# Kernel optimization log

Hardware: AMD Instinct MI355X
Metric: run time of the kernel (lower is better)

The kernel has to match this reference:

```python
import jax, jax.numpy as jnp
import numpy as np

E = 500000       # number of temporal edges
D = 128          # in_feats
DOUT = 128       # out_feats
N_NODES = 50000  # destination node vocabulary


def setup_inputs() -> dict:
    key = jax.random.key(0)
    k = jax.random.split(key, 6)
    src_feat = jax.random.normal(k[0], (E, D), jnp.float32)
    dst_feat = jax.random.normal(k[1], (E, D), jnp.float32)
    # edges sorted by destination node (and implicitly by timestamp within each bucket)
    dst = jnp.sort(jax.random.randint(k[2], (E,), 0, N_NODES))
    W_self = jax.random.normal(k[3], (D, DOUT), jnp.float32) / np.sqrt(D).astype(np.float32)
    b_self = jnp.zeros((DOUT,), jnp.float32)
    W_neigh = jax.random.normal(k[4], (D, DOUT), jnp.float32) / np.sqrt(D).astype(np.float32)
    b_neigh = jnp.zeros((DOUT,), jnp.float32)
    return dict(src_feat=src_feat, dst_feat=dst_feat, dst=dst,
                W_self=W_self, b_self=b_self, W_neigh=W_neigh, b_neigh=b_neigh)


def _segment_cummean(feat, dst):
    """Cumulative mean of `feat` within contiguous buckets of equal `dst`.

    Equivalent to DGL group_apply_edges(group_by='dst') with the 'mean' branch:
    h_feat = cumsum(h_neighs, dim=1) / (deg_index + 1) on the ragged buckets.
    """
    En = feat.shape[0]
    idx = jnp.arange(En)
    is_start = jnp.concatenate([jnp.ones((1,), bool), dst[1:] != dst[:-1]])
    # running max propagates each bucket's start index to all of its edges
    start_idx = jax.lax.associative_scan(jnp.maximum, jnp.where(is_start, idx, 0))
    cs = jnp.cumsum(feat, axis=0)  # [E, D] global prefix sum
    base = jnp.where((start_idx > 0)[:, None],
                     cs[jnp.maximum(start_idx - 1, 0)], jnp.float32(0.0))
    seg_cs = cs - base                       # within-bucket inclusive cumsum
    pos = (idx - start_idx).astype(feat.dtype)
    return seg_cs / (pos + 1.0)[:, None]     # cumulative mean


def reference(src_feat, dst_feat, dst, W_self, b_self, W_neigh, b_neigh):
    h_neigh = _segment_cummean(src_feat, dst)
    # rst = fc_self(h_self) + fc_neigh(mask_feat)
    return (dst_feat @ W_self + b_self) + (h_neigh @ W_neigh + b_neigh)
```

## Files before the change

### kernel.cpp

```cpp
#include <hip/hip_runtime.h>

typedef float f32x4 __attribute__((ext_vector_type(4)));
typedef __bf16 bf16x8 __attribute__((ext_vector_type(8)));

typedef __attribute__((address_space(3))) unsigned char lds_u8;
typedef __attribute__((address_space(1))) const unsigned char g_u8c;

__device__ __forceinline__ unsigned short f2bf(float f) {
  unsigned int u = __float_as_uint(f);
  u += 0x7FFFu + ((u >> 16) & 1u);
  return (unsigned short)(u >> 16);
}
__device__ __forceinline__ unsigned int pk2(float a, float b) {
  return (unsigned int)f2bf(a) | ((unsigned int)f2bf(b) << 16);
}
__device__ __forceinline__ void gload16(const void* g, void* l) {
  __builtin_amdgcn_global_load_lds((g_u8c*)g, (lds_u8*)l, 16, 0, 0);
}

__global__ void k_prep(const float* __restrict__ Ws, const float* __restrict__ Wn,
                       const float* __restrict__ bs, const float* __restrict__ bn,
                       unsigned short* __restrict__ wt, float* __restrict__ bias) {
  int idx = blockIdx.x * 256 + threadIdx.x;
  int n = idx >> 8, k = idx & 255;
  float v = (k < 128) ? Ws[k * 128 + n] : Wn[(k - 128) * 128 + n];
  int ct = n >> 4, l15 = n & 15, kt = k >> 5, lg = (k >> 3) & 3, j = k & 7;
  wt[(((kt << 3) | ct) << 9) + (((lg << 4) | l15) << 3) + j] = f2bf(v);
  if (idx < 128) bias[idx] = bs[idx] + bn[idx];
}

__global__ __launch_bounds__(256, 4) void k_fused(
    const float* __restrict__ src, const float* __restrict__ dstf,
    const int* __restrict__ dst, const unsigned short* __restrict__ wt,
    const float* __restrict__ bias, float* __restrict__ out, int E)
{
  __shared__ __align__(16) unsigned char slab[4][8192];
  const int lane = threadIdx.x & 63, wid = threadIdx.x >> 6;
  const int l15 = lane & 15, lg = lane >> 4;

  const int nwg = gridDim.x, bid = blockIdx.x;
  const int q = nwg >> 3, r = nwg & 7;
  const int xcd = bid & 7, ix = bid >> 3;
  const int swb = (xcd < r ? xcd * (q + 1) : r * (q + 1) + (xcd - r) * q) + ix;

  const long e0 = ((long)swb * 4 + wid) * 16;
  if (e0 >= E) return;
  const long emax = (long)E - 1;
  unsigned char* ssrc = slab[wid];

  long rc = e0 + l15; if (rc > emax) rc = emax;
  int dcur = dst[rc];
  long rp = rc - 1; if (rp < 0) rp = 0;
  int dprev = dst[rp];
  long back = e0 - 1 - lane;
  long backc = back < 0 ? 0 : back;
  int bd = dst[backc];

  #pragma unroll
  for (int i = 0; i < 8; ++i) {
    int r2 = i * 2 + (lane >> 5);
    long gr = e0 + r2; if (gr > emax) gr = emax;
    int colb = ((lane & 31) << 4) ^ ((r2 & 7) << 5);
    gload16((const char*)src + gr * 512 + colb, ssrc + i * 1024);
  }

  unsigned mask16 = (unsigned)(__ballot((rc > 0) && (dcur != dprev)) & 0xFFFFull);

  int d0 = __shfl(dcur, 0);
  unsigned long long m = __ballot((back >= 0) && (bd == d0));
  unsigned long long nm = ~m;
  int L = (nm == 0ull) ? 64 : __builtin_ctzll(nm);
  long s = e0 - L;
  while (s > 0 && dst[s - 1] == d0) --s;

  float ax = 0.f, ay = 0.f;
  long e = s;
  while (e < e0) {
    int nb = (int)(e0 - e); if (nb > 8) nb = 8;
    float2 t[8];
    #pragma unroll
    for (int j = 0; j < 8; ++j)
      if (j < nb) t[j] = *(const float2*)(src + (e + j) * 128 + lane * 2);
    #pragma unroll
    for (int j = 0; j < 8; ++j)
      if (j < nb) { ax += t[j].x; ay += t[j].y; }
    e += nb;
  }
  int pos = (int)(e0 - s);

  asm volatile("s_waitcnt vmcnt(0)" ::: "memory");

  #pragma unroll
  for (int rr = 0; rr < 16; ++rr) {
    if (mask16 & (1u << rr)) { ax = 0.f; ay = 0.f; pos = 0; }
    float2 v = *(const float2*)(ssrc + rr * 512 + ((lane * 8) ^ ((rr & 7) << 5)));
    ax += v.x; ay += v.y;
    float inv = __builtin_amdgcn_rcpf((float)(pos + 1));
    *(unsigned int*)(ssrc + rr * 512 + ((lane * 4) ^ ((rr & 7) << 4))) = pk2(ax * inv, ay * inv);
    ++pos;
  }

  asm volatile("s_waitcnt lgkmcnt(0)" ::: "memory");

  long arow = e0 + l15; if (arow > emax) arow = emax;
  const float* ap = dstf + arow * 128 + lg * 8;
  float4 af[8];
  #pragma unroll
  for (int kt = 0; kt < 4; ++kt) {
    af[kt * 2]     = *(const float4*)(ap + kt * 32);
    af[kt * 2 + 1] = *(const float4*)(ap + kt * 32 + 4);
  }

  f32x4 acc[8];
  #pragma unroll
  for (int ct = 0; ct < 8; ++ct) acc[ct] = (f32x4){0.f, 0.f, 0.f, 0.f};
  float bcol[8];
  #pragma unroll
  for (int ct = 0; ct < 8; ++ct) bcol[ct] = bias[ct * 16 + l15];

  #pragma unroll
  for (int kt = 0; kt < 8; ++kt) {
    bf16x8 a;
    if (kt < 4) {
      float4 x = af[kt * 2], y = af[kt * 2 + 1];
      union { unsigned int u[4]; bf16x8 v; } cv;
      cv.u[0] = pk2(x.x, x.y); cv.u[1] = pk2(x.z, x.w);
      cv.u[2] = pk2(y.x, y.y); cv.u[3] = pk2(y.z, y.w);
      a = cv.v;
    } else {
      a = *(const bf16x8*)(ssrc + l15 * 512 + ((((kt - 4) * 64) + lg * 16) ^ ((l15 & 7) << 4)));
    }
    bf16x8 b[8];
    #pragma unroll
    for (int ct = 0; ct < 8; ++ct)
      b[ct] = *(const bf16x8*)(wt + (((kt << 3) | ct) << 9) + (lane << 3));
    #pragma unroll
    for (int ct = 0; ct < 8; ++ct)
      acc[ct] = __builtin_amdgcn_mfma_f32_16x16x32_bf16(a, b[ct], acc[ct], 0, 0, 0);
  }

  #pragma unroll
  for (int i = 0; i < 4; ++i) {
    long row = e0 + lg * 4 + i;
    if (row < E) {
      float* op = out + row * 128 + l15;
      #pragma unroll
      for (int ct = 0; ct < 8; ++ct) op[ct * 16] = acc[ct][i] + bcol[ct];
    }
  }
}

extern "C" void kernel_launch(void* const* d_in, const int* in_sizes, int n_in,
                              void* d_out, int out_size, void* d_ws, size_t ws_size,
                              hipStream_t stream) {
  const float* src_feat = (const float*)d_in[0];
  const float* dst_feat = (const float*)d_in[1];
  const int*   dst      = (const int*)d_in[2];
  const float* W_self   = (const float*)d_in[3];
  const float* b_self   = (const float*)d_in[4];
  const float* W_neigh  = (const float*)d_in[5];
  const float* b_neigh  = (const float*)d_in[6];
  float* out = (float*)d_out;
  const int E = in_sizes[2];

  unsigned short* wt   = (unsigned short*)d_ws;
  float*          bias = (float*)((char*)d_ws + 65536);

  k_prep<<<128, 256, 0, stream>>>(W_self, W_neigh, b_self, b_neigh, wt, bias);

  int blocks = (E + 63) / 64;
  k_fused<<<blocks, 256, 0, stream>>>(src_feat, dst_feat, dst, wt, bias, out, E);
}
```

Baseline: 212.6 us.

## Make each workgroup loop over a 256-edge span with register-resident weights

Each workgroup now processes a contiguous span of 256 edges in 32-row tiles, not 64 edges once. Each wave keeps its 32-column slice of the bf16 weight matrix in registers for the whole span, so weights are no longer reloaded per tile. Both src and dst features are streamed into LDS with async global-to-LDS loads, and the next tile's loads are issued before the current tile's MFMAs. The cross-tile segment prefix carries over, so the backward scan for a segment start runs once per span instead of once per 16-row wave. The cost is fewer workgroups, an extra __syncthreads per tile, and only half of each wave doing the serial cumulative-mean pass.

```diff
diff --git a/kernel.cpp b/kernel.cpp
--- a/kernel.cpp
+++ b/kernel.cpp
@@ -18,134 +18,168 @@
   __builtin_amdgcn_global_load_lds((g_u8c*)g, (lds_u8*)l, 16, 0, 0);
 }
 
+#define SPAN 256
+
 __global__ void k_prep(const float* __restrict__ Ws, const float* __restrict__ Wn,
                        const float* __restrict__ bs, const float* __restrict__ bn,
-                       unsigned short* __restrict__ wt, float* __restrict__ bias) {
+                       unsigned short* __restrict__ wt2, float* __restrict__ bias) {
   int idx = blockIdx.x * 256 + threadIdx.x;
   int n = idx >> 8, k = idx & 255;
   float v = (k < 128) ? Ws[k * 128 + n] : Wn[(k - 128) * 128 + n];
-  int ct = n >> 4, l15 = n & 15, kt = k >> 5, lg = (k >> 3) & 3, j = k & 7;
-  wt[(((kt << 3) | ct) << 9) + (((lg << 4) | l15) << 3) + j] = f2bf(v);
+  int w = n >> 5, c2 = (n >> 4) & 1, l15 = n & 15;
+  int kt = k >> 5, lg = (k >> 3) & 3, j = k & 7;
+  wt2[(((w * 16 + kt * 2 + c2) * 64) + lg * 16 + l15) * 8 + j] = f2bf(v);
   if (idx < 128) bias[idx] = bs[idx] + bn[idx];
 }
 
-__global__ __launch_bounds__(256, 4) void k_fused(
+__global__ __launch_bounds__(256) void k_fused(
     const float* __restrict__ src, const float* __restrict__ dstf,
-    const int* __restrict__ dst, const unsigned short* __restrict__ wt,
-    const float* __restrict__ bias, float* __restrict__ out, int E)
+    const int* __restrict__ dst, const unsigned short* __restrict__ wt2,
+    const float* __restrict__ bias, float* __restrict__ out, int E, int nwg)
 {
-  __shared__ __align__(16) unsigned char slab[4][8192];
+  __shared__ __align__(16) unsigned char sbuf[32 * 512];
+  __shared__ __align__(16) unsigned char dbuf[32 * 512];
+  __shared__ __align__(16) unsigned char hbuf[32 * 256];
+
   const int lane = threadIdx.x & 63, wid = threadIdx.x >> 6;
-  const int l15 = lane & 15, lg = lane >> 4;
-
-  const int nwg = gridDim.x, bid = blockIdx.x;
+  const int l15 = lane & 15, lg = lane >> 4, l31 = lane & 31;
+  const long emax = (long)E - 1;
+
+  const int bid = blockIdx.x;
   const int q = nwg >> 3, r = nwg & 7;
   const int xcd = bid & 7, ix = bid >> 3;
   const int swb = (xcd < r ? xcd * (q + 1) : r * (q + 1) + (xcd - r) * q) + ix;
 
-  const long e0 = ((long)swb * 4 + wid) * 16;
-  if (e0 >= E) return;
-  const long emax = (long)E - 1;
-  unsigned char* ssrc = slab[wid];
-
-  long rc = e0 + l15; if (rc > emax) rc = emax;
-  int dcur = dst[rc];
-  long rp = rc - 1; if (rp < 0) rp = 0;
-  int dprev = dst[rp];
-  long back = e0 - 1 - lane;
+  const long W0 = (long)swb * SPAN;
+  const long Wend = (W0 + SPAN < (long)E) ? W0 + SPAN : (long)E;
+  const int nt = (int)((Wend - W0 + 31) >> 5);
+
+  bf16x8 b[16];
+  #pragma unroll
+  for (int f = 0; f < 16; ++f)
+    b[f] = *(const bf16x8*)(wt2 + ((wid * 16 + f) * 64 + lane) * 8);
+  const float bc0 = bias[wid * 32 + l15];
+  const float bc1 = bias[wid * 32 + 16 + l15];
+
+  const int mycol = wid * 32 + l31;
+
+  int d0 = dst[W0];
+  long back = W0 - 1 - lane;
   long backc = back < 0 ? 0 : back;
   int bd = dst[backc];
-
-  #pragma unroll
-  for (int i = 0; i < 8; ++i) {
-    int r2 = i * 2 + (lane >> 5);
-    long gr = e0 + r2; if (gr > emax) gr = emax;
-    int colb = ((lane & 31) << 4) ^ ((r2 & 7) << 5);
-    gload16((const char*)src + gr * 512 + colb, ssrc + i * 1024);
-  }
-
-  unsigned mask16 = (unsigned)(__ballot((rc > 0) && (dcur != dprev)) & 0xFFFFull);
-
-  int d0 = __shfl(dcur, 0);
   unsigned long long m = __ballot((back >= 0) && (bd == d0));
   unsigned long long nm = ~m;
   int L = (nm == 0ull) ? 64 : __builtin_ctzll(nm);
-  long s = e0 - L;
+  long s = W0 - L;
   while (s > 0 && dst[s - 1] == d0) --s;
-
-  float ax = 0.f, ay = 0.f;
-  long e = s;
-  while (e < e0) {
-    int nb = (int)(e0 - e); if (nb > 8) nb = 8;
-    float2 t[8];
+  float ax = 0.f;
+  if (lane < 32) {
+    long e = s;
+    while (e < W0) {
+      int nb = (int)(W0 - e); if (nb > 8) nb = 8;
+      float tv[8];
+      #pragma unroll
+      for (int j2 = 0; j2 < 8; ++j2)
+        if (j2 < nb) tv[j2] = src[(e + j2) * 128 + mycol];
+      #pragma unroll
+      for (int j2 = 0; j2 < 8; ++j2)
+        if (j2 < nb) ax += tv[j2];
+      e += nb;
+    }
+  }
+  int pos = (int)(W0 - s);
+
+  #pragma unroll
+  for (int qd = 0; qd < 4; ++qd) {
+    int i = wid * 4 + qd;
+    int r2 = i * 2 + (lane >> 5);
+    long gr = W0 + r2; if (gr > emax) gr = emax;
+    int colb = (l31 << 4) ^ ((r2 & 7) << 5);
+    gload16((const char*)src + gr * 512 + colb, sbuf + i * 1024);
+    gload16((const char*)dstf + gr * 512 + colb, dbuf + i * 1024);
+  }
+
+  for (int t = 0; t < nt; ++t) {
+    const long tb = W0 + (long)t * 32;
+
+    long rc = tb + l31; if (rc > emax) rc = emax;
+    int dcur = dst[rc];
+    long rp = rc - 1; if (rp < 0) rp = 0;
+    int dprev = dst[rp];
+
+    __syncthreads();
+
+    unsigned mask = (unsigned)__ballot((lane < 32) && (rc > 0) && (dcur != dprev));
+
+    if (lane < 32) {
+      #pragma unroll
+      for (int rr = 0; rr < 32; ++rr) {
+        if ((mask >> rr) & 1u) { ax = 0.f; pos = 0; }
+        float v = *(const float*)(sbuf + rr * 512 + ((mycol * 4) ^ ((rr & 7) << 5)));
+        ax += v;
+        float mean = ax * __builtin_amdgcn_rcpf((float)(pos + 1));
+        *(unsigned short*)(hbuf + rr * 256 + ((mycol * 2) ^ ((rr & 7) << 4))) = f2bf(mean);
+        ++pos;
+      }
+    }
+
+    __syncthreads();
+
+    bf16x8 abf[2][4];
     #pragma unroll
-    for (int j = 0; j < 8; ++j)
-      if (j < nb) t[j] = *(const float2*)(src + (e + j) * 128 + lane * 2);
+    for (int rt = 0; rt < 2; ++rt) {
+      int row = rt * 16 + l15;
+      #pragma unroll
+      for (int kt = 0; kt < 4; ++kt) {
+        const unsigned char* p = dbuf + row * 512 + ((kt * 128 + lg * 32) ^ ((row & 7) << 5));
+        float4 x = *(const float4*)p;
+        float4 y = *(const float4*)(p + 16);
+        union { unsigned int u[4]; bf16x8 v; } cv;
+        cv.u[0] = pk2(x.x, x.y); cv.u[1] = pk2(x.z, x.w);
+        cv.u[2] = pk2(y.x, y.y); cv.u[3] = pk2(y.z, y.w);
+        abf[rt][kt] = cv.v;
+      }
+    }
+
+    __syncthreads();
+
+    if (t + 1 < nt) {
+      const long nb2 = tb + 32;
+      #pragma unroll
+      for (int qd = 0; qd < 4; ++qd) {
+        int i = wid * 4 + qd;
+        int r2 = i * 2 + (lane >> 5);
+        long gr = nb2 + r2; if (gr > emax) gr = emax;
+        int colb = (l31 << 4) ^ ((r2 & 7) << 5);
+        gload16((const char*)src + gr * 512 + colb, sbuf + i * 1024);
+        gload16((const char*)dstf + gr * 512 + colb, dbuf + i * 1024);
+      }
+    }
+
     #pragma unroll
-    for (int j = 0; j < 8; ++j)
-      if (j < nb) { ax += t[j].x; ay += t[j].y; }
-    e += nb;
-  }
-  int pos = (int)(e0 - s);
-
-  asm volatile("s_waitcnt vmcnt(0)" ::: "memory");
-
-  #pragma unroll
-  for (int rr = 0; rr < 16; ++rr) {
-    if (mask16 & (1u << rr)) { ax = 0.f; ay = 0.f; pos = 0; }
-    float2 v = *(const float2*)(ssrc + rr * 512 + ((lane * 8) ^ ((rr & 7) << 5)));
-    ax += v.x; ay += v.y;
-    float inv = __builtin_amdgcn_rcpf((float)(pos + 1));
-    *(unsigned int*)(ssrc + rr * 512 + ((lane * 4) ^ ((rr & 7) << 4))) = pk2(ax * inv, ay * inv);
-    ++pos;
-  }
-
-  asm volatile("s_waitcnt lgkmcnt(0)" ::: "memory");
-
-  long arow = e0 + l15; if (arow > emax) arow = emax;
-  const float* ap = dstf + arow * 128 + lg * 8;
-  float4 af[8];
-  #pragma unroll
-  for (int kt = 0; kt < 4; ++kt) {
-    af[kt * 2]     = *(const float4*)(ap + kt * 32);
-    af[kt * 2 + 1] = *(const float4*)(ap + kt * 32 + 4);
-  }
-
-  f32x4 acc[8];
-  #pragma unroll
-  for (int ct = 0; ct < 8; ++ct) acc[ct] = (f32x4){0.f, 0.f, 0.f, 0.f};
-  float bcol[8];
-  #pragma unroll
-  for (int ct = 0; ct < 8; ++ct) bcol[ct] = bias[ct * 16 + l15];
-
-  #pragma unroll
-  for (int kt = 0; kt < 8; ++kt) {
-    bf16x8 a;
-    if (kt < 4) {
-      float4 x = af[kt * 2], y = af[kt * 2 + 1];
-      union { unsigned int u[4]; bf16x8 v; } cv;
-      cv.u[0] = pk2(x.x, x.y); cv.u[1] = pk2(x.z, x.w);
-      cv.u[2] = pk2(y.x, y.y); cv.u[3] = pk2(y.z, y.w);
-      a = cv.v;
-    } else {
-      a = *(const bf16x8*)(ssrc + l15 * 512 + ((((kt - 4) * 64) + lg * 16) ^ ((l15 & 7) << 4)));
-    }
-    bf16x8 b[8];
-    #pragma unroll
-    for (int ct = 0; ct < 8; ++ct)
-      b[ct] = *(const bf16x8*)(wt + (((kt << 3) | ct) << 9) + (lane << 3));
-    #pragma unroll
-    for (int ct = 0; ct < 8; ++ct)
-      acc[ct] = __builtin_amdgcn_mfma_f32_16x16x32_bf16(a, b[ct], acc[ct], 0, 0, 0);
-  }
-
-  #pragma unroll
-  for (int i = 0; i < 4; ++i) {
-    long row = e0 + lg * 4 + i;
-    if (row < E) {
-      float* op = out + row * 128 + l15;
-      #pragma unroll
-      for (int ct = 0; ct < 8; ++ct) op[ct * 16] = acc[ct][i] + bcol[ct];
+    for (int rt = 0; rt < 2; ++rt) {
+      int row = rt * 16 + l15;
+      f32x4 a0 = {0.f, 0.f, 0.f, 0.f}, a1 = {0.f, 0.f, 0.f, 0.f};
+      #pragma unroll
+      for (int kt = 0; kt < 8; ++kt) {
+        bf16x8 a;
+        if (kt < 4) {
+          a = abf[rt][kt];
+        } else {
+          a = *(const bf16x8*)(hbuf + row * 256 + ((((kt - 4) * 64) + lg * 16) ^ ((row & 7) << 4)));
+        }
+        a0 = __builtin_amdgcn_mfma_f32_16x16x32_bf16(a, b[kt * 2 + 0], a0, 0, 0, 0);
+        a1 = __builtin_amdgcn_mfma_f32_16x16x32_bf16(a, b[kt * 2 + 1], a1, 0, 0, 0);
+      }
+      #pragma unroll
+      for (int i = 0; i < 4; ++i) {
+        long row2 = tb + rt * 16 + lg * 4 + i;
+        if (row2 < E) {
+          float* op = out + row2 * 128 + wid * 32 + l15;
+          op[0]  = a0[i] + bc0;
+          op[16] = a1[i] + bc1;
+        }
+      }
     }
   }
 }
@@ -163,11 +197,11 @@
   float* out = (float*)d_out;
   const int E = in_sizes[2];
 
-  unsigned short* wt   = (unsigned short*)d_ws;
-  float*          bias = (float*)((char*)d_ws + 65536);
-
-  k_prep<<<128, 256, 0, stream>>>(W_self, W_neigh, b_self, b_neigh, wt, bias);
-
-  int blocks = (E + 63) / 64;
-  k_fused<<<blocks, 256, 0, stream>>>(src_feat, dst_feat, dst, wt, bias, out, E);
-}
+  unsigned short* wt2  = (unsigned short*)d_ws;
+  float*          bias = (float*)((char*)d_ws + 131072);
+
+  k_prep<<<128, 256, 0, stream>>>(W_self, W_neigh, b_self, b_neigh, wt2, bias);
+
+  int nwg = (E + SPAN - 1) / SPAN;
+  k_fused<<<nwg, 256, 0, stream>>>(src_feat, dst_feat, dst, wt2, bias, out, E, nwg);
+}
```

After: 175.7 us. 1.21x faster.

## Apply neighbor projection before segmented prefix mean via masked MFMA scan

Applied to the files above, without the earlier changes.

The kernel now uses linearity to project src rows through W_neigh first, then does the within-bucket cumulative sum on the projected outputs. The sum is a bf16 MFMA against a 0/1 lower-triangular segment mask, with a carry passed across 32-row tiles. Each block covers a 256-edge span and each of its 8 waves owns 16 output columns, so a wave loops over the span sequentially instead of handling one 16-row tile. This removes the per-row LDS scan and the global_load_lds staging. In exchange, every wave rereads the full src and dst rows for its column slice, and the projected values are rounded to bf16 before accumulation.

```diff
diff --git a/kernel.cpp b/kernel.cpp
--- a/kernel.cpp
+++ b/kernel.cpp
@@ -2,20 +2,17 @@
 
 typedef float f32x4 __attribute__((ext_vector_type(4)));
 typedef __bf16 bf16x8 __attribute__((ext_vector_type(8)));
-
-typedef __attribute__((address_space(3))) unsigned char lds_u8;
-typedef __attribute__((address_space(1))) const unsigned char g_u8c;
 
 __device__ __forceinline__ unsigned short f2bf(float f) {
   unsigned int u = __float_as_uint(f);
   u += 0x7FFFu + ((u >> 16) & 1u);
   return (unsigned short)(u >> 16);
 }
-__device__ __forceinline__ unsigned int pk2(float a, float b) {
-  return (unsigned int)f2bf(a) | ((unsigned int)f2bf(b) << 16);
-}
-__device__ __forceinline__ void gload16(const void* g, void* l) {
-  __builtin_amdgcn_global_load_lds((g_u8c*)g, (lds_u8*)l, 16, 0, 0);
+__device__ __forceinline__ bf16x8 cvt8(float4 x, float4 y) {
+  bf16x8 r;
+  r[0] = (__bf16)x.x; r[1] = (__bf16)x.y; r[2] = (__bf16)x.z; r[3] = (__bf16)x.w;
+  r[4] = (__bf16)y.x; r[5] = (__bf16)y.y; r[6] = (__bf16)y.z; r[7] = (__bf16)y.w;
+  return r;
 }
 
 __global__ void k_prep(const float* __restrict__ Ws, const float* __restrict__ Wn,
@@ -29,124 +26,167 @@
   if (idx < 128) bias[idx] = bs[idx] + bn[idx];
 }
 
-__global__ __launch_bounds__(256, 4) void k_fused(
+#define SPAN 256
+
+__global__ __launch_bounds__(512, 4) void k_fused(
     const float* __restrict__ src, const float* __restrict__ dstf,
     const int* __restrict__ dst, const unsigned short* __restrict__ wt,
-    const float* __restrict__ bias, float* __restrict__ out, int E)
+    const float* __restrict__ bias, float* __restrict__ out, int E, int nwg)
 {
-  __shared__ __align__(16) unsigned char slab[4][8192];
+  __shared__ __align__(16) unsigned char ylds[8][1280];
+  __shared__ float cbuf[8][128];
   const int lane = threadIdx.x & 63, wid = threadIdx.x >> 6;
-  const int l15 = lane & 15, lg = lane >> 4;
-
-  const int nwg = gridDim.x, bid = blockIdx.x;
+  const int l15 = lane & 15, lg = lane >> 4, l31 = lane & 31;
+  const long emax = (long)E - 1;
+
+  const int bid = blockIdx.x;
   const int q = nwg >> 3, r = nwg & 7;
   const int xcd = bid & 7, ix = bid >> 3;
   const int swb = (xcd < r ? xcd * (q + 1) : r * (q + 1) + (xcd - r) * q) + ix;
 
-  const long e0 = ((long)swb * 4 + wid) * 16;
-  if (e0 >= E) return;
-  const long emax = (long)E - 1;
-  unsigned char* ssrc = slab[wid];
-
-  long rc = e0 + l15; if (rc > emax) rc = emax;
-  int dcur = dst[rc];
-  long rp = rc - 1; if (rp < 0) rp = 0;
-  int dprev = dst[rp];
-  long back = e0 - 1 - lane;
+  const long W0 = (long)swb * SPAN;
+  if (W0 >= E) return;
+  const long Wend = (W0 + SPAN < (long)E) ? W0 + SPAN : (long)E;
+  const int nt = (int)((Wend - W0 + 31) >> 5);
+
+  unsigned char* yw = ylds[wid];
+  float* cw = cbuf[wid];
+  const float bc = bias[wid * 16 + l15];
+
+  int d0 = dst[W0];
+  long back = W0 - 1 - lane;
   long backc = back < 0 ? 0 : back;
   int bd = dst[backc];
-
-  #pragma unroll
-  for (int i = 0; i < 8; ++i) {
-    int r2 = i * 2 + (lane >> 5);
-    long gr = e0 + r2; if (gr > emax) gr = emax;
-    int colb = ((lane & 31) << 4) ^ ((r2 & 7) << 5);
-    gload16((const char*)src + gr * 512 + colb, ssrc + i * 1024);
+  unsigned long long mm = __ballot((back >= 0) && (bd == d0));
+  unsigned long long nmm = ~mm;
+  int L = (nmm == 0ull) ? 64 : __builtin_ctzll(nmm);
+  long s = W0 - L;
+  while (s > 0 && dst[s - 1] == d0) --s;
+  int pos0 = (int)(W0 - s);
+
+  float carry = 0.f;
+  if (pos0 > 0) {
+    float px = 0.f, py = 0.f;
+    for (long e = s; e < W0; ) {
+      int nb = (int)(W0 - e); if (nb > 8) nb = 8;
+      float2 tv[8];
+      #pragma unroll
+      for (int j = 0; j < 8; ++j)
+        if (j < nb) tv[j] = *(const float2*)(src + (e + j) * 128 + lane * 2);
+      #pragma unroll
+      for (int j = 0; j < 8; ++j)
+        if (j < nb) { px += tv[j].x; py += tv[j].y; }
+      e += nb;
+    }
+    cw[lane * 2] = px; cw[lane * 2 + 1] = py;
+    asm volatile("s_waitcnt lgkmcnt(0)" ::: "memory");
+    f32x4 accc = {0.f, 0.f, 0.f, 0.f};
+    #pragma unroll
+    for (int kt = 0; kt < 4; ++kt) {
+      float4 x = {0,0,0,0}, y = {0,0,0,0};
+      if (l15 == 0) {
+        x = *(const float4*)(cw + kt * 32 + lg * 8);
+        y = *(const float4*)(cw + kt * 32 + lg * 8 + 4);
+      }
+      bf16x8 a = cvt8(x, y);
+      bf16x8 b = *(const bf16x8*)(wt + ((((kt + 4) << 3) | wid) << 9) + (lane << 3));
+      accc = __builtin_amdgcn_mfma_f32_16x16x32_bf16(a, b, accc, 0, 0, 0);
+    }
+    carry = __shfl(accc[0], l15);
   }
 
-  unsigned mask16 = (unsigned)(__ballot((rc > 0) && (dcur != dprev)) & 0xFFFFull);
-
-  int d0 = __shfl(dcur, 0);
-  unsigned long long m = __ballot((back >= 0) && (bd == d0));
-  unsigned long long nm = ~m;
-  int L = (nm == 0ull) ? 64 : __builtin_ctzll(nm);
-  long s = e0 - L;
-  while (s > 0 && dst[s - 1] == d0) --s;
-
-  float ax = 0.f, ay = 0.f;
-  long e = s;
-  while (e < e0) {
-    int nb = (int)(e0 - e); if (nb > 8) nb = 8;
-    float2 t[8];
-    #pragma unroll
-    for (int j = 0; j < 8; ++j)
-      if (j < nb) t[j] = *(const float2*)(src + (e + j) * 128 + lane * 2);
-    #pragma unroll
-    for (int j = 0; j < 8; ++j)
-      if (j < nb) { ax += t[j].x; ay += t[j].y; }
-    e += nb;
-  }
-  int pos = (int)(e0 - s);
-
-  asm volatile("s_waitcnt vmcnt(0)" ::: "memory");
-
-  #pragma unroll
-  for (int rr = 0; rr < 16; ++rr) {
-    if (mask16 & (1u << rr)) { ax = 0.f; ay = 0.f; pos = 0; }
-    float2 v = *(const float2*)(ssrc + rr * 512 + ((lane * 8) ^ ((rr & 7) << 5)));
-    ax += v.x; ay += v.y;
-    float inv = __builtin_amdgcn_rcpf((float)(pos + 1));
-    *(unsigned int*)(ssrc + rr * 512 + ((lane * 4) ^ ((rr & 7) << 4))) = pk2(ax * inv, ay * inv);
-    ++pos;
-  }
-
-  asm volatile("s_waitcnt lgkmcnt(0)" ::: "memory");
-
-  long arow = e0 + l15; if (arow > emax) arow = emax;
-  const float* ap = dstf + arow * 128 + lg * 8;
-  float4 af[8];
-  #pragma unroll
-  for (int kt = 0; kt < 4; ++kt) {
-    af[kt * 2]     = *(const float4*)(ap + kt * 32);
-    af[kt * 2 + 1] = *(const float4*)(ap + kt * 32 + 4);
-  }
-
-  f32x4 acc[8];
-  #pragma unroll
-  for (int ct = 0; ct < 8; ++ct) acc[ct] = (f32x4){0.f, 0.f, 0.f, 0.f};
-  float bcol[8];
-  #pragma unroll
-  for (int ct = 0; ct < 8; ++ct) bcol[ct] = bias[ct * 16 + l15];
-
-  #pragma unroll
-  for (int kt = 0; kt < 8; ++kt) {
-    bf16x8 a;
-    if (kt < 4) {
-      float4 x = af[kt * 2], y = af[kt * 2 + 1];
-      union { unsigned int u[4]; bf16x8 v; } cv;
-      cv.u[0] = pk2(x.x, x.y); cv.u[1] = pk2(x.z, x.w);
-      cv.u[2] = pk2(y.x, y.y); cv.u[3] = pk2(y.z, y.w);
-      a = cv.v;
-    } else {
-      a = *(const bf16x8*)(ssrc + l15 * 512 + ((((kt - 4) * 64) + lg * 16) ^ ((l15 & 7) << 4)));
-    }
-    bf16x8 b[8];
-    #pragma unroll
-    for (int ct = 0; ct < 8; ++ct)
-      b[ct] = *(const bf16x8*)(wt + (((kt << 3) | ct) << 9) + (lane << 3));
-    #pragma unroll
-    for (int ct = 0; ct < 8; ++ct)
-      acc[ct] = __builtin_amdgcn_mfma_f32_16x16x32_bf16(a, b[ct], acc[ct], 0, 0, 0);
-  }
-
-  #pragma unroll
-  for (int i = 0; i < 4; ++i) {
-    long row = e0 + lg * 4 + i;
-    if (row < E) {
-      float* op = out + row * 128 + l15;
-      #pragma unroll
-      for (int ct = 0; ct < 8; ++ct) op[ct * 16] = acc[ct][i] + bcol[ct];
-    }
+  for (int t = 0; t < nt; ++t) {
+    const long tb = W0 + (long)t * 32;
+
+    long rc = tb + l31; if (rc > emax) rc = emax;
+    int dcur = dst[rc];
+    long rp = rc - 1; if (rp < 0) rp = 0;
+    int dprev = dst[rp];
+    unsigned mask = (unsigned)(__ballot((lane < 32) && (rc > 0) && (dcur != dprev)));
+
+    bf16x8 aS[2][4], aD[2][4];
+    #pragma unroll
+    for (int rt = 0; rt < 2; ++rt) {
+      long row = tb + rt * 16 + l15; if (row > emax) row = emax;
+      const float* ps = src + row * 128 + lg * 8;
+      const float* pd = dstf + row * 128 + lg * 8;
+      #pragma unroll
+      for (int kt = 0; kt < 4; ++kt) {
+        float4 sx = *(const float4*)(ps + kt * 32);
+        float4 sy = *(const float4*)(ps + kt * 32 + 4);
+        float4 dx = *(const float4*)(pd + kt * 32);
+        float4 dy = *(const float4*)(pd + kt * 32 + 4);
+        aS[rt][kt] = cvt8(sx, sy);
+        aD[rt][kt] = cvt8(dx, dy);
+      }
+    }
+
+    f32x4 accO[2] = {{0,0,0,0},{0,0,0,0}};
+    f32x4 accY[2] = {{0,0,0,0},{0,0,0,0}};
+    #pragma unroll
+    for (int kt = 0; kt < 4; ++kt) {
+      bf16x8 bS = *(const bf16x8*)(wt + (((kt << 3) | wid) << 9) + (lane << 3));
+      bf16x8 bN = *(const bf16x8*)(wt + ((((kt + 4) << 3) | wid) << 9) + (lane << 3));
+      #pragma unroll
+      for (int rt = 0; rt < 2; ++rt) {
+        accO[rt] = __builtin_amdgcn_mfma_f32_16x16x32_bf16(aD[rt][kt], bS, accO[rt], 0, 0, 0);
+        accY[rt] = __builtin_amdgcn_mfma_f32_16x16x32_bf16(aS[rt][kt], bN, accY[rt], 0, 0, 0);
+      }
+    }
+
+    #pragma unroll
+    for (int rt = 0; rt < 2; ++rt) {
+      unsigned lo = (unsigned)f2bf(accY[rt][0]) | ((unsigned)f2bf(accY[rt][1]) << 16);
+      unsigned hi = (unsigned)f2bf(accY[rt][2]) | ((unsigned)f2bf(accY[rt][3]) << 16);
+      *(unsigned long long*)(yw + l15 * 80 + rt * 32 + lg * 8) =
+          (unsigned long long)lo | ((unsigned long long)hi << 32);
+    }
+    asm volatile("s_waitcnt lgkmcnt(0)" ::: "memory");
+
+    bf16x8 Mf[2];
+    #pragma unroll
+    for (int rt = 0; rt < 2; ++rt) {
+      int rr = rt * 16 + l15;
+      unsigned bits = mask & (0xFFFFFFFFu >> (31 - rr));
+      int sr = (bits == 0) ? 0 : (31 - __clz(bits));
+      union { unsigned u[4]; bf16x8 v; } mu;
+      #pragma unroll
+      for (int p = 0; p < 4; ++p) {
+        int e0 = lg * 8 + p * 2;
+        unsigned lo = (e0 >= sr && e0 <= rr) ? 0x3F80u : 0u;
+        unsigned hi = (e0 + 1 >= sr && e0 + 1 <= rr) ? 0x3F80u : 0u;
+        mu.u[p] = lo | (hi << 16);
+      }
+      Mf[rt] = mu.v;
+    }
+
+    bf16x8 yb = *(const bf16x8*)(yw + l15 * 80 + lg * 16);
+    f32x4 accZ[2] = {{0,0,0,0},{0,0,0,0}};
+    #pragma unroll
+    for (int rt = 0; rt < 2; ++rt)
+      accZ[rt] = __builtin_amdgcn_mfma_f32_16x16x32_bf16(Mf[rt], yb, accZ[rt], 0, 0, 0);
+
+    float z31 = __shfl(accZ[1][3], 48 + l15);
+
+    #pragma unroll
+    for (int rt = 0; rt < 2; ++rt) {
+      #pragma unroll
+      for (int i = 0; i < 4; ++i) {
+        int rr = rt * 16 + lg * 4 + i;
+        unsigned bits = mask & (0xFFFFFFFFu >> (31 - rr));
+        float cnt, u;
+        if (bits == 0) { cnt = (float)(rr + 1 + pos0); u = 1.f; }
+        else { cnt = (float)(rr - (31 - __clz(bits)) + 1); u = 0.f; }
+        float inv = __builtin_amdgcn_rcpf(cnt);
+        long grow = tb + rr;
+        if (grow < E)
+          out[grow * 128 + wid * 16 + l15] =
+              accO[rt][i] + bc + (accZ[rt][i] + u * carry) * inv;
+      }
+    }
+
+    if (mask == 0) { carry += z31; pos0 += 32; }
+    else           { carry  = z31; pos0  = __clz(mask) + 1; }
   }
 }
 
@@ -168,6 +208,6 @@
 
   k_prep<<<128, 256, 0, stream>>>(W_self, W_neigh, b_self, b_neigh, wt, bias);
 
-  int blocks = (E + 63) / 64;
-  k_fused<<<blocks, 256, 0, stream>>>(src_feat, dst_feat, dst, wt, bias, out, E);
-}
+  int nwg = (E + SPAN - 1) / SPAN;
+  k_fused<<<nwg, 512, 0, stream>>>(src_feat, dst_feat, dst, wt, bias, out, E, nwg);
+}
```

Result: slower. 533.7 us (+151.1%).
